# Performance work log

Hardware: AMD Instinct MI355X
Metric: run time of the kernel (lower is better)

The kernel has to match this reference:

```python
import jax, jax.numpy as jnp
import numpy as np

B, S, D, NH = 4, 2048, 768, 12
DK = D // NH  # 64


def setup_inputs() -> dict:
    key = jax.random.key(0)
    ks = jax.random.split(key, 5)
    scale = 1.0 / np.sqrt(D)
    return {
        "x": jax.random.normal(ks[0], (B, S, D), dtype=jnp.float32),
        "Wq": jax.random.normal(ks[1], (D, D), dtype=jnp.float32) * scale,
        "Wk": jax.random.normal(ks[2], (D, D), dtype=jnp.float32) * scale,
        "Wv": jax.random.normal(ks[3], (D, D), dtype=jnp.float32) * scale,
        "W0": jax.random.normal(ks[4], (D, D), dtype=jnp.float32) * scale,
    }


def reference(x, Wq, Wk, Wv, W0):
    b, s, d = x.shape
    # nn.Linear(d, d, bias=False): y = x @ W.T
    q = (x @ Wq.T).reshape(b, s, NH, DK)
    k = (x @ Wk.T).reshape(b, s, NH, DK)
    v = (x @ Wv.T).reshape(b, s, NH, DK)
    scores = jnp.einsum('bqhd,bkhd->bhqk', q, k) / np.sqrt(DK)
    # Faithful to source: softmax over dim=2 (the QUERY axis), no mask.
    attn = jax.nn.softmax(scores, axis=2)
    heads = jnp.einsum('bhqk,bkhd->bhqd', attn, v)
    # Faithful to source: direct reshape (b,h,q,d) -> (b,s,d_m), no transpose.
    out = heads.reshape(b, s, d) @ W0.T
    return out
```

## Files before the change

kernel.cpp:

```cpp
#include <hip/hip_runtime.h>
#include <hip/hip_bf16.h>
#include <stdint.h>
#include <math.h>

#define NB  4
#define NS  2048
#define ND  768
#define NHD 12
#define NDK 64
#define NBH (NB*NHD)

#define QSCALE 0.180336879f

typedef short short8 __attribute__((ext_vector_type(8)));
typedef float f32x4  __attribute__((ext_vector_type(4)));
typedef float f32x16 __attribute__((ext_vector_type(16)));
typedef unsigned int uint2v __attribute__((ext_vector_type(2)));

#define MFMA16(a,b,c) __builtin_amdgcn_mfma_f32_16x16x32_bf16(a,b,c,0,0,0)
#define MFMA32(a,b,c) __builtin_amdgcn_mfma_f32_32x32x16_bf16(a,b,c,0,0,0)

extern "C" __device__ float __ocml_native_exp2_f32(float);
__device__ __forceinline__ float nexp2(float x){ return __ocml_native_exp2_f32(x); }

__device__ __forceinline__ short f2b(float f){
  union { float f; uint32_t u; } v; v.f = f;
  uint32_t u = v.u + 0x7fffu + ((v.u >> 16) & 1u);
  return (short)(u >> 16);
}
__device__ __forceinline__ float b2f(short s){
  union { float f; uint32_t u; } v; v.u = ((uint32_t)(unsigned short)s) << 16; return v.f;
}
__device__ __forceinline__ uint32_t cvtpk(float lo, float hi){
  uint32_t r;
  asm("v_cvt_pk_bf16_f32 %0, %1, %2" : "=v"(r) : "v"(lo), "v"(hi));
  return r;
}
__device__ __forceinline__ short8 mk8(uint32_t a, uint32_t b, uint32_t c, uint32_t d){
  union { uint32_t u[4]; short8 v; } x;
  x.u[0]=a; x.u[1]=b; x.u[2]=c; x.u[3]=d; return x.v;
}
__device__ __forceinline__ void pack2(const float* p, short8& o0, short8& o1){
  uint32_t x0 = cvtpk(p[0], p[1]),  x1 = cvtpk(p[2], p[3]);
  uint32_t y0 = cvtpk(p[4], p[5]),  y1 = cvtpk(p[6], p[7]);
  uint2v r02 = __builtin_amdgcn_permlane32_swap(x0, y0, false, false);
  uint2v r13 = __builtin_amdgcn_permlane32_swap(x1, y1, false, false);
  o0 = mk8(r02.x, r13.x, r02.y, r13.y);
  uint32_t x2 = cvtpk(p[8],  p[9]),  x3 = cvtpk(p[10], p[11]);
  uint32_t y2 = cvtpk(p[12], p[13]), y3 = cvtpk(p[14], p[15]);
  uint2v r46 = __builtin_amdgcn_permlane32_swap(x2, y2, false, false);
  uint2v r57 = __builtin_amdgcn_permlane32_swap(x3, y3, false, false);
  o1 = mk8(r46.x, r57.x, r46.y, r57.y);
}

__device__ __forceinline__ void gload16(const void* g, void* lds){
  __builtin_amdgcn_global_load_lds(
      (const __attribute__((address_space(1))) uint32_t*)g,
      (__attribute__((address_space(3))) uint32_t*)lds, 16, 0, 0);
}

__global__ __launch_bounds__(256) void cast_all(const float* __restrict__ x,
    const float* __restrict__ wq, const float* __restrict__ wk,
    const float* __restrict__ wv, const float* __restrict__ w0,
    short* __restrict__ xb, short* __restrict__ wqb, short* __restrict__ wkb,
    short* __restrict__ wvb, short* __restrict__ w0b){
  const int NX = NB*NS*ND/8;
  const int NW = ND*ND/8;
  int i = blockIdx.x*256 + threadIdx.x;
  const float* src; short* dst; int off;
  if (i < NX){ src = x; dst = xb; off = i; }
  else {
    int j = i - NX; int wsel = j / NW; off = j - wsel*NW;
    src = (wsel==0)?wq:((wsel==1)?wk:((wsel==2)?wv:w0));
    dst = (wsel==0)?wqb:((wsel==1)?wkb:((wsel==2)?wvb:w0b));
  }
  const f32x4* p = (const f32x4*)(src + (size_t)off*8);
  f32x4 v0 = p[0], v1 = p[1];
  short8 r;
  r[0]=f2b(v0[0]); r[1]=f2b(v0[1]); r[2]=f2b(v0[2]); r[3]=f2b(v0[3]);
  r[4]=f2b(v1[0]); r[5]=f2b(v1[1]); r[6]=f2b(v1[2]); r[7]=f2b(v1[3]);
  *(short8*)(dst + (size_t)off*8) = r;
}

__device__ __forceinline__ void gemm128_core(const short* __restrict__ A,
                                             const short* __restrict__ Bw,
                                             int rowA0, int rowB0,
                                             short* As, short* Bs, f32x4 acc[4][4]){
  const int t = threadIdx.x;
  const int l  = t & 63;
  const int wm = ((t >> 7) & 1) * 64;
  const int wn = ((t >> 6) & 1) * 64;
  const int lr = l & 15, lg = l >> 4;
  #pragma unroll
  for (int mt=0; mt<4; ++mt)
    #pragma unroll
    for (int nt=0; nt<4; ++nt) acc[mt][nt] = (f32x4){0.f,0.f,0.f,0.f};

  #pragma unroll
  for (int c = 0; c < 4; ++c){
    int u  = c*256 + t;
    int m  = u >> 3;
    int kb = ((u & 7) << 4) ^ ((m & 7) << 4);
    gload16((const char*)(A  + (size_t)(rowA0 + m)*768) + kb,
            (char*)As + ((c*256 + (t & 0xC0)) << 4));
    gload16((const char*)(Bw + (size_t)(rowB0 + m)*768) + kb,
            (char*)Bs + ((c*256 + (t & 0xC0)) << 4));
  }
  __syncthreads();

  for (int kt = 0; kt < 12; ++kt){
    const int cur = (kt & 1) * (128*64);
    const int nxt = ((kt + 1) & 1) * (128*64);
    if (kt < 11){
      #pragma unroll
      for (int c = 0; c < 4; ++c){
        int u  = c*256 + t;
        int m  = u >> 3;
        int kb = ((u & 7) << 4) ^ ((m & 7) << 4);
        gload16((const char*)(A  + (size_t)(rowA0 + m)*768 + (kt+1)*64) + kb,
                (char*)(As + nxt) + ((c*256 + (t & 0xC0)) << 4));
        gload16((const char*)(Bw + (size_t)(rowB0 + m)*768 + (kt+1)*64) + kb,
                (char*)(Bs + nxt) + ((c*256 + (t & 0xC0)) << 4));
      }
    }
    short8 af[4][2], bf[4][2];
    #pragma unroll
    for (int mt=0; mt<4; ++mt)
      #pragma unroll
      for (int ks=0; ks<2; ++ks){
        int m  = wm + mt*16 + lr;
        int kb = (ks*32 + lg*8) * 2;
        af[mt][ks] = *(const short8*)((const char*)(As + cur) + ((m*128 + kb) ^ ((m & 7) << 4)));
        int n  = wn + mt*16 + lr;
        bf[mt][ks] = *(const short8*)((const char*)(Bs + cur) + ((n*128 + kb) ^ ((n & 7) << 4)));
      }
    #pragma unroll
    for (int mt=0; mt<4; ++mt)
      #pragma unroll
      for (int nt=0; nt<4; ++nt){
        acc[mt][nt] = MFMA16(af[mt][0], bf[nt][0], acc[mt][nt]);
        acc[mt][nt] = MFMA16(af[mt][1], bf[nt][1], acc[mt][nt]);
      }
    __syncthreads();
  }
}

__global__ __launch_bounds__(256) void gemm_qkv(const short* __restrict__ Xb,
    const short* __restrict__ Wqb, const short* __restrict__ Wkb, const short* __restrict__ Wvb,
    short* __restrict__ Qf, short* __restrict__ Kf, short* __restrict__ V){
  __shared__ __align__(16) short As[2*128*64];
  __shared__ __align__(16) short Bs[2*128*64];
  const int wsel = blockIdx.y / 6;
  const int nb   = (blockIdx.y % 6) * 128;
  const short* W = (wsel==0) ? Wqb : ((wsel==1) ? Wkb : Wvb);
  f32x4 acc[4][4];
  gemm128_core(Xb, W, blockIdx.x*128, nb, As, Bs, acc);
  const int t = threadIdx.x, l = t & 63;
  const int wm = ((t>>7)&1)*64, wn = ((t>>6)&1)*64;
  const int lr = l & 15, lg = l >> 4;
  if (wsel == 2){
    #pragma unroll
    for (int mt=0; mt<4; ++mt)
      #pragma unroll
      for (int nt=0; nt<4; ++nt)
        #pragma unroll
        for (int r=0; r<4; ++r){
          int m = blockIdx.x*128 + wm + mt*16 + lg*4 + r;
          int n = nb + wn + nt*16 + lr;
          V[(size_t)m*768 + n] = f2b(acc[mt][nt][r]);
        }
  } else {
    short* O = (wsel==0) ? Qf : Kf;
    const float scl = (wsel==0) ? QSCALE : 1.0f;
    const int bh = (blockIdx.x >> 4)*NHD + ((nb + wn) >> 6);
    const int s0 = (blockIdx.x & 15)*128 + wm;
    short* Ob = O + (size_t)bh*131072;
    #pragma unroll
    for (int mt=0; mt<4; ++mt)
      #pragma unroll
      for (int nt=0; nt<4; ++nt)
        #pragma unroll
        for (int r=0; r<4; ++r){
          int s  = s0 + mt*16 + lg*4 + r;
          int dk = nt*16 + lr;
          Ob[(size_t)((s>>5)*4 + (dk>>4))*512 + ((dk>>3)&1)*256 + (s&31)*8 + (dk&7)]
            = f2b(acc[mt][nt][r] * scl);
        }
  }
}

__global__ __launch_bounds__(256) void gemm_out(const short* __restrict__ Hb,
    const short* __restrict__ W0b, float* __restrict__ out){
  __shared__ __align__(16) short As[2*128*64];
  __shared__ __align__(16) short Bs[2*128*64];
  const int nb = blockIdx.y * 128;
  f32x4 acc[4][4];
  gemm128_core(Hb, W0b, blockIdx.x*128, nb, As, Bs, acc);
  const int t = threadIdx.x, l = t & 63;
  const int wm = ((t>>7)&1)*64, wn = ((t>>6)&1)*64;
  const int lr = l & 15, lg = l >> 4;
  #pragma unroll
  for (int mt=0; mt<4; ++mt)
    #pragma unroll
    for (int nt=0; nt<4; ++nt)
      #pragma unroll
      for (int r=0; r<4; ++r){
        int m = blockIdx.x*128 + wm + mt*16 + lg*4 + r;
        int n = nb + wn + nt*16 + lr;
        out[(size_t)m*768 + n] = acc[mt][nt][r];
      }
}

__global__ __launch_bounds__(256, 3) void pass_a(const short* __restrict__ Qf,
                                                 const short* __restrict__ Kf,
                                                 float* __restrict__ invs){
  __shared__ float redA[2][4][32];
  const int t = threadIdx.x, w = t >> 6, l = t & 63;
  const int lq = l & 31, hf = l >> 5;
  const int linear = blockIdx.y * 32 + blockIdx.x;
  const int c8 = linear & 7, j = linear >> 3;
  const int bh = c8 * 6 + (j >> 5);
  const int kp = j & 31;

  const short8* KgA = (const short8*)(Kf + ((size_t)bh*64 + kp*2    )*2048);
  const short8* KgB = (const short8*)(Kf + ((size_t)bh*64 + kp*2 + 1)*2048);
  short8 kfA[4], kfB[4];
  #pragma unroll
  for (int c=0; c<4; ++c){ kfA[c] = KgA[c*64 + l]; kfB[c] = KgB[c*64 + l]; }

  float psA[16], psB[16];
  #pragma unroll
  for (int r=0; r<16; ++r){ psA[r] = 0.f; psB[r] = 0.f; }

  const short8* Qb = (const short8*)(Qf + (size_t)bh*131072);
  for (int qt = w*16; qt < w*16 + 16; ++qt){
    const short8* Qg = Qb + qt*256;
    short8 q0 = Qg[l], q1 = Qg[64+l], q2 = Qg[128+l], q3 = Qg[192+l];
    {
      f32x16 cA = {};
      cA = MFMA32(kfA[0], q0, cA);
      cA = MFMA32(kfA[1], q1, cA);
      cA = MFMA32(kfA[2], q2, cA);
      cA = MFMA32(kfA[3], q3, cA);
      #pragma unroll
      for (int r=0; r<16; ++r) psA[r] += nexp2(cA[r]);
    }
    {
      f32x16 cB = {};
      cB = MFMA32(kfB[0], q0, cB);
      cB = MFMA32(kfB[1], q1, cB);
      cB = MFMA32(kfB[2], q2, cB);
      cB = MFMA32(kfB[3], q3, cB);
      #pragma unroll
      for (int r=0; r<16; ++r) psB[r] += nexp2(cB[r]);
    }
  }
  #pragma unroll
  for (int r=0; r<16; ++r){
    float a = psA[r], b = psB[r];
    a += __shfl_xor(a, 1); a += __shfl_xor(a, 2);
    a += __shfl_xor(a, 4); a += __shfl_xor(a, 8); a += __shfl_xor(a, 16);
    b += __shfl_xor(b, 1); b += __shfl_xor(b, 2);
    b += __shfl_xor(b, 4); b += __shfl_xor(b, 8); b += __shfl_xor(b, 16);
    if (lq == 0){
      int kr = (r&3) + 8*(r>>2) + 4*hf;
      redA[0][w][kr] = a;
      redA[1][w][kr] = b;
    }
  }
  __syncthreads();
  if (t < 64){
    int kvt = t >> 5, kr = t & 31;
    float s = redA[kvt][0][kr] + redA[kvt][1][kr] + redA[kvt][2][kr] + redA[kvt][3][kr];
    invs[(size_t)bh*NS + (kp*2 + kvt)*32 + kr] = 1.0f / s;
  }
}

__global__ __launch_bounds__(256) void pack_v(const short* __restrict__ V,
                                              const float* __restrict__ invs,
                                              short* __restrict__ Vf){
  __shared__ short tile[64][66];
  const int sb = blockIdx.x * 64;
  const int bh = blockIdx.y;
  const int b = bh / NHD, h = bh % NHD;
  const int t = threadIdx.x;
  {
    int r = t >> 2, dkb = (t & 3) * 16;
    float iv = invs[(size_t)bh*NS + sb + r];
    const short* src = V + ((size_t)(b*NS + sb + r)*NHD + h)*NDK + dkb;
    short8 v0 = *(const short8*)src;
    short8 v1 = *(const short8*)(src + 8);
    #pragma unroll
    for (int j=0;j<8;++j) tile[r][dkb+j]   = f2b(b2f(v0[j]) * iv);
    #pragma unroll
    for (int j=0;j<8;++j) tile[r][dkb+8+j] = f2b(b2f(v1[j]) * iv);
  }
  __syncthreads();
  {
    const int c = t >> 6, l = t & 63;
    const int lq = l & 31, hf = l >> 5;
    const int dk = (c>>1)*32 + lq;
    #pragma unroll
    for (int kt_l = 0; kt_l < 2; ++kt_l){
      int kv0 = kt_l*32 + (c&1)*16 + hf*8;
      short8 o;
      #pragma unroll
      for (int j=0;j<8;++j) o[j] = tile[kv0+j][dk];
      *(short8*)(Vf + (((size_t)bh*64 + (sb>>5) + kt_l)*256 + c*64 + l)*8) = o;
    }
  }
}

__device__ __forceinline__ void reduce_store(float (&red)[2][32][64],
                                             f32x16& a0, f32x16& a1,
                                             int w, int l, int lq, int hf,
                                             short* __restrict__ Hd,
                                             size_t bhNS, int qt){
  if (w >= 2){
    #pragma unroll
    for (int r=0; r<16; ++r){ red[w-2][r][l] = a0[r]; red[w-2][16+r][l] = a1[r]; }
  }
  __syncthreads();
  if (w < 2){
    #pragma unroll
    for (int r=0; r<16; ++r){ a0[r] += red[w][r][l]; a1[r] += red[w][16+r][l]; }
  }
  __syncthreads();
  if (w == 1){
    #pragma unroll
    for (int r=0; r<16; ++r){ red[0][r][l] = a0[r]; red[0][16+r][l] = a1[r]; }
  }
  __syncthreads();
  if (w == 0){
    #pragma unroll
    for (int r=0; r<16; ++r){
      a0[r] += red[0][r][l];
      a1[r] += red[0][16+r][l];
      int q = qt*32 + (r&3) + 8*(r>>2) + 4*hf;
      short* dst = Hd + (bhNS + q)*NDK;
      dst[lq]      = f2b(a0[r]);
      dst[32 + lq] = f2b(a1[r]);
    }
  }
}

__global__ __launch_bounds__(256, 3) void pass_c(const short* __restrict__ Qf,
                                                 const short* __restrict__ Kf,
                                                 const short* __restrict__ Vf,
                                                 short* __restrict__ Hd){
  __shared__ float red[2][32][64];
  const int t = threadIdx.x, w = t >> 6, l = t & 63;
  const int lq = l & 31, hf = l >> 5;
  const int linear = blockIdx.y * 32 + blockIdx.x;
  const int c8 = linear & 7, j = linear >> 3;
  const int bh = c8 * 6 + (j >> 5);
  const int qp = j & 31;

  const short8* QgA = (const short8*)(Qf + ((size_t)bh*64 + qp*2    )*2048);
  const short8* QgB = (const short8*)(Qf + ((size_t)bh*64 + qp*2 + 1)*2048);
  short8 qfA[4], qfB[4];
  #pragma unroll
  for (int c=0; c<4; ++c){ qfA[c] = QgA[c*64 + l]; qfB[c] = QgB[c*64 + l]; }

  const short8* Kb = (const short8*)(Kf + (size_t)bh*131072);
  const short8* Vb = (const short8*)(Vf + (size_t)bh*131072);

  f32x16 accA0 = {}, accA1 = {}, accB0 = {}, accB1 = {};

  for (int kt = w*16; kt < w*16 + 16; ++kt){
    const short8* Kg = Kb + kt*256;
    const short8* Vg = Vb + kt*256;
    short8 k0 = Kg[l], k1 = Kg[64+l], k2 = Kg[128+l], k3 = Kg[192+l];
    short8 v0 = Vg[l], v1 = Vg[64+l], v2 = Vg[128+l], v3 = Vg[192+l];

    {
      f32x16 cA = {};
      cA = MFMA32(k0, qfA[0], cA);
      cA = MFMA32(k1, qfA[1], cA);
      cA = MFMA32(k2, qfA[2], cA);
      cA = MFMA32(k3, qfA[3], cA);
      float pA[16];
      #pragma unroll
      for (int r=0; r<16; ++r) pA[r] = nexp2(cA[r]);
      short8 paA0, paA1;
      pack2(pA, paA0, paA1);
      accA0 = MFMA32(paA0, v0, accA0);
      accA0 = MFMA32(paA1, v1, accA0);
      accA1 = MFMA32(paA0, v2, accA1);
      accA1 = MFMA32(paA1, v3, accA1);
    }
    {
      f32x16 cB = {};
      cB = MFMA32(k0, qfB[0], cB);
      cB = MFMA32(k1, qfB[1], cB);
      cB = MFMA32(k2, qfB[2], cB);
      cB = MFMA32(k3, qfB[3], cB);
      float pB[16];
      #pragma unroll
      for (int r=0; r<16; ++r) pB[r] = nexp2(cB[r]);
      short8 paB0, paB1;
      pack2(pB, paB0, paB1);
      accB0 = MFMA32(paB0, v0, accB0);
      accB0 = MFMA32(paB1, v1, accB0);
      accB1 = MFMA32(paB0, v2, accB1);
      accB1 = MFMA32(paB1, v3, accB1);
    }
  }

  const size_t bhNS = (size_t)bh*NS;
  reduce_store(red, accA0, accA1, w, l, lq, hf, Hd, bhNS, qp*2);
  __syncthreads();
  reduce_store(red, accB0, accB1, w, l, lq, hf, Hd, bhNS, qp*2 + 1);
}

extern "C" void kernel_launch(void* const* d_in, const int* in_sizes, int n_in,
                              void* d_out, int out_size, void* d_ws, size_t ws_size,
                              hipStream_t stream){
  (void)in_sizes; (void)n_in; (void)out_size; (void)ws_size;
  const float* x  = (const float*)d_in[0];
  const float* Wq = (const float*)d_in[1];
  const float* Wk = (const float*)d_in[2];
  const float* Wv = (const float*)d_in[3];
  const float* W0 = (const float*)d_in[4];

  char* ws = (char*)d_ws;
  const size_t SZ_X = (size_t)NB*NS*ND*2;
  const size_t SZ_W = (size_t)ND*ND*2;
  short* Xb   = (short*)(ws);
  short* Wqb  = (short*)(ws + SZ_X);
  short* Wkb  = (short*)(ws + SZ_X + 1*SZ_W);
  short* Wvb  = (short*)(ws + SZ_X + 2*SZ_W);
  short* W0b  = (short*)(ws + SZ_X + 3*SZ_W);
  short* Qf   = (short*)(ws + 1*SZ_X + 4*SZ_W);
  short* Kf   = (short*)(ws + 2*SZ_X + 4*SZ_W);
  short* V    = (short*)(ws + 3*SZ_X + 4*SZ_W);
  short* Vf   = (short*)(ws + 4*SZ_X + 4*SZ_W);
  float* invs = (float*)(ws + 5*SZ_X + 4*SZ_W);
  short* Hd   = Xb;
  float* out  = (float*)d_out;

  cast_all<<<dim3(4224), dim3(256), 0, stream>>>(x, Wq, Wk, Wv, W0,
                                                 Xb, Wqb, Wkb, Wvb, W0b);

  gemm_qkv<<<dim3(64,18), dim3(256), 0, stream>>>(Xb, Wqb, Wkb, Wvb, Qf, Kf, V);
  pass_a<<<dim3(32,48), dim3(256), 0, stream>>>(Qf, Kf, invs);
  pack_v<<<dim3(32,48), dim3(256), 0, stream>>>(V, invs, Vf);
  pass_c<<<dim3(32,48), dim3(256), 0, stream>>>(Qf, Kf, Vf, Hd);
  gemm_out<<<dim3(64,6), dim3(256), 0, stream>>>(Hd, W0b, out);
}
```

Baseline: 164.9 us.

## Pre-pack X and QKV weights into MFMA fragment layout, drop LDS staging

The cast kernel now writes X and Wq/Wk/Wv in a fragment-packed bf16 layout, so each wave lane can load its MFMA operand directly from global memory as one 16-byte vector. The QKV GEMM no longer stages tiles through shared memory or synchronises, and reads operands straight into registers per k-step. This removes LDS traffic and barriers but gives up LDS reuse and double-buffered prefetch. Each operand fragment is re-read from global memory and L2 by several waves, with no overlap between loads and MFMAs beyond what the compiler schedules.

Measured after the change: 233.1 us. 41.4% more time.

```diff
diff --git a/kernel.cpp b/kernel.cpp
--- a/kernel.cpp
+++ b/kernel.cpp
@@ -59,27 +59,41 @@
       (__attribute__((address_space(3))) uint32_t*)lds, 16, 0, 0);
 }
 
+__device__ __forceinline__ size_t packed_idx(int m, int c0){
+  int g = (((m >> 7)*12 + (c0 >> 6))*16) + (((m >> 4) & 7)*2) + ((c0 >> 5) & 1);
+  return (size_t)g*512 + (size_t)((((c0 >> 3) & 3)*16) + (m & 15))*8;
+}
+
 __global__ __launch_bounds__(256) void cast_all(const float* __restrict__ x,
     const float* __restrict__ wq, const float* __restrict__ wk,
     const float* __restrict__ wv, const float* __restrict__ w0,
-    short* __restrict__ xb, short* __restrict__ wqb, short* __restrict__ wkb,
-    short* __restrict__ wvb, short* __restrict__ w0b){
+    short* __restrict__ xf, short* __restrict__ wqf, short* __restrict__ wkf,
+    short* __restrict__ wvf, short* __restrict__ w0b){
   const int NX = NB*NS*ND/8;
   const int NW = ND*ND/8;
   int i = blockIdx.x*256 + threadIdx.x;
-  const float* src; short* dst; int off;
-  if (i < NX){ src = x; dst = xb; off = i; }
+  const float* src; short* dst; int off; bool packed;
+  if (i < NX){ src = x; dst = xf; off = i; packed = true; }
   else {
     int j = i - NX; int wsel = j / NW; off = j - wsel*NW;
     src = (wsel==0)?wq:((wsel==1)?wk:((wsel==2)?wv:w0));
-    dst = (wsel==0)?wqb:((wsel==1)?wkb:((wsel==2)?wvb:w0b));
+    dst = (wsel==0)?wqf:((wsel==1)?wkf:((wsel==2)?wvf:w0b));
+    packed = (wsel != 3);
   }
   const f32x4* p = (const f32x4*)(src + (size_t)off*8);
   f32x4 v0 = p[0], v1 = p[1];
   short8 r;
   r[0]=f2b(v0[0]); r[1]=f2b(v0[1]); r[2]=f2b(v0[2]); r[3]=f2b(v0[3]);
   r[4]=f2b(v1[0]); r[5]=f2b(v1[1]); r[6]=f2b(v1[2]); r[7]=f2b(v1[3]);
-  *(short8*)(dst + (size_t)off*8) = r;
+  size_t didx;
+  if (packed){
+    int m  = off / 96;
+    int c0 = (off % 96) * 8;
+    didx = packed_idx(m, c0);
+  } else {
+    didx = (size_t)off * 8;
+  }
+  *(short8*)(dst + didx) = r;
 }
 
 __device__ __forceinline__ void gemm128_core(const short* __restrict__ A,
@@ -145,18 +159,45 @@
   }
 }
 
-__global__ __launch_bounds__(256) void gemm_qkv(const short* __restrict__ Xb,
-    const short* __restrict__ Wqb, const short* __restrict__ Wkb, const short* __restrict__ Wvb,
+__global__ __launch_bounds__(256) void gemm_qkv(const short* __restrict__ Xf,
+    const short* __restrict__ Wqf, const short* __restrict__ Wkf, const short* __restrict__ Wvf,
     short* __restrict__ Qf, short* __restrict__ Kf, short* __restrict__ V){
-  __shared__ __align__(16) short As[2*128*64];
-  __shared__ __align__(16) short Bs[2*128*64];
   const int wsel = blockIdx.y / 6;
   const int nb   = (blockIdx.y % 6) * 128;
-  const short* W = (wsel==0) ? Wqb : ((wsel==1) ? Wkb : Wvb);
+  const int rtw  = blockIdx.y % 6;
+  const int xt   = blockIdx.x;
+  const short8* Ag = (const short8*)Xf;
+  const short8* Bg = (const short8*)((wsel==0) ? Wqf : ((wsel==1) ? Wkf : Wvf));
+  const int t = threadIdx.x, l = t & 63;
+  const int wm4 = ((t>>7)&1)*4, wn4 = ((t>>6)&1)*4;
+
   f32x4 acc[4][4];
-  gemm128_core(Xb, W, blockIdx.x*128, nb, As, Bs, acc);
-  const int t = threadIdx.x, l = t & 63;
-  const int wm = ((t>>7)&1)*64, wn = ((t>>6)&1)*64;
+  #pragma unroll
+  for (int mt=0; mt<4; ++mt)
+    #pragma unroll
+    for (int nt=0; nt<4; ++nt) acc[mt][nt] = (f32x4){0.f,0.f,0.f,0.f};
+
+  for (int kt = 0; kt < 12; ++kt){
+    short8 af[4][2], bf[4][2];
+    const int ga = (xt*12 + kt)*16;
+    const int gb = (rtw*12 + kt)*16;
+    #pragma unroll
+    for (int mt=0; mt<4; ++mt)
+      #pragma unroll
+      for (int ks=0; ks<2; ++ks){
+        af[mt][ks] = Ag[(size_t)(ga + (wm4+mt)*2 + ks)*64 + l];
+        bf[mt][ks] = Bg[(size_t)(gb + (wn4+mt)*2 + ks)*64 + l];
+      }
+    #pragma unroll
+    for (int mt=0; mt<4; ++mt)
+      #pragma unroll
+      for (int nt=0; nt<4; ++nt){
+        acc[mt][nt] = MFMA16(af[mt][0], bf[nt][0], acc[mt][nt]);
+        acc[mt][nt] = MFMA16(af[mt][1], bf[nt][1], acc[mt][nt]);
+      }
+  }
+
+  const int wm = wm4*16, wn = wn4*16;
   const int lr = l & 15, lg = l >> 4;
   if (wsel == 2){
     #pragma unroll
@@ -165,15 +206,15 @@
       for (int nt=0; nt<4; ++nt)
         #pragma unroll
         for (int r=0; r<4; ++r){
-          int m = blockIdx.x*128 + wm + mt*16 + lg*4 + r;
+          int m = xt*128 + wm + mt*16 + lg*4 + r;
           int n = nb + wn + nt*16 + lr;
           V[(size_t)m*768 + n] = f2b(acc[mt][nt][r]);
         }
   } else {
     short* O = (wsel==0) ? Qf : Kf;
     const float scl = (wsel==0) ? QSCALE : 1.0f;
-    const int bh = (blockIdx.x >> 4)*NHD + ((nb + wn) >> 6);
-    const int s0 = (blockIdx.x & 15)*128 + wm;
+    const int bh = (xt >> 4)*NHD + ((nb + wn) >> 6);
+    const int s0 = (xt & 15)*128 + wm;
     short* Ob = O + (size_t)bh*131072;
     #pragma unroll
     for (int mt=0; mt<4; ++mt)
@@ -426,23 +467,23 @@
   char* ws = (char*)d_ws;
   const size_t SZ_X = (size_t)NB*NS*ND*2;
   const size_t SZ_W = (size_t)ND*ND*2;
-  short* Xb   = (short*)(ws);
-  short* Wqb  = (short*)(ws + SZ_X);
-  short* Wkb  = (short*)(ws + SZ_X + 1*SZ_W);
-  short* Wvb  = (short*)(ws + SZ_X + 2*SZ_W);
+  short* Xf   = (short*)(ws);
+  short* Wqf  = (short*)(ws + SZ_X);
+  short* Wkf  = (short*)(ws + SZ_X + 1*SZ_W);
+  short* Wvf  = (short*)(ws + SZ_X + 2*SZ_W);
   short* W0b  = (short*)(ws + SZ_X + 3*SZ_W);
   short* Qf   = (short*)(ws + 1*SZ_X + 4*SZ_W);
   short* Kf   = (short*)(ws + 2*SZ_X + 4*SZ_W);
   short* V    = (short*)(ws + 3*SZ_X + 4*SZ_W);
   short* Vf   = (short*)(ws + 4*SZ_X + 4*SZ_W);
   float* invs = (float*)(ws + 5*SZ_X + 4*SZ_W);
-  short* Hd   = Xb;
+  short* Hd   = Xf;
   float* out  = (float*)d_out;
 
   cast_all<<<dim3(4224), dim3(256), 0, stream>>>(x, Wq, Wk, Wv, W0,
-                                                 Xb, Wqb, Wkb, Wvb, W0b);
-
-  gemm_qkv<<<dim3(64,18), dim3(256), 0, stream>>>(Xb, Wqb, Wkb, Wvb, Qf, Kf, V);
+                                                 Xf, Wqf, Wkf, Wvf, W0b);
+
+  gemm_qkv<<<dim3(64,18), dim3(256), 0, stream>>>(Xf, Wqf, Wkf, Wvf, Qf, Kf, V);
   pass_a<<<dim3(32,48), dim3(256), 0, stream>>>(Qf, Kf, invs);
   pack_v<<<dim3(32,48), dim3(256), 0, stream>>>(V, invs, Vf);
   pass_c<<<dim3(32,48), dim3(256), 0, stream>>>(Qf, Kf, Vf, Hd);
```
